# Kernel tuning notes

Measured on AMD Instinct MI355X. Metric: run time of the kernel, lower is better.

Reference implementation:

```python
import jax, jax.numpy as jnp
import numpy as np

N_NODES = 100000
N_EDGES = 1600000
D = 128


def setup_inputs() -> dict:
    key = jax.random.key(0)
    ks = jax.random.split(key, 10)
    s = 1.0 / np.sqrt(D)
    return {
        "feat": jax.random.normal(ks[0], (N_NODES, D), dtype=jnp.float32),
        "W_self0": jax.random.normal(ks[1], (D, D), dtype=jnp.float32) * s,
        "W_neigh0": jax.random.normal(ks[2], (D, D), dtype=jnp.float32) * s,
        "b0": jnp.zeros((D,), dtype=jnp.float32),
        "W_self1": jax.random.normal(ks[3], (D, D), dtype=jnp.float32) * s,
        "W_neigh1": jax.random.normal(ks[4], (D, D), dtype=jnp.float32) * s,
        "b1": jnp.zeros((D,), dtype=jnp.float32),
        "ln_g": jnp.ones((D,), dtype=jnp.float32),
        "ln_b": jnp.zeros((D,), dtype=jnp.float32),
        "edge_src": jax.random.randint(ks[5], (N_EDGES,), 0, N_NODES, dtype=jnp.int32),
        "edge_dst": jax.random.randint(ks[6], (N_EDGES,), 0, N_NODES, dtype=jnp.int32),
        "in_deg": jax.random.randint(ks[7], (N_NODES,), 1, 64, dtype=jnp.int32),
    }


def _sage_layer(h, src, dst, inv_deg, W_self, W_neigh, b):
    # mean aggregation over incoming neighbors: gather -> segment_sum -> scale
    msg = jax.ops.segment_sum(h[src], dst, num_segments=N_NODES)  # [N, d]
    h_neigh = msg * inv_deg[:, None]
    return h @ W_self + h_neigh @ W_neigh + b


def _layer_norm(x, g, b, eps=1e-5):
    mu = jnp.mean(x, axis=-1, keepdims=True)
    var = jnp.mean((x - mu) ** 2, axis=-1, keepdims=True)
    return (x - mu) * jax.lax.rsqrt(var + eps) * g + b


def reference(feat, W_self0, W_neigh0, b0, W_self1, W_neigh1, b1, ln_g, ln_b,
              edge_src, edge_dst, in_deg):
    # Eval mode: dropout = identity, no EmbeddingSelector / reg loss.
    inv_deg = 1.0 / jnp.maximum(in_deg, 1).astype(feat.dtype)
    h = _sage_layer(feat, edge_src, edge_dst, inv_deg, W_self0, W_neigh0, b0)
    h = _layer_norm(h, ln_g, ln_b)
    h = jax.nn.relu(h)
    h = _sage_layer(h, edge_src, edge_dst, inv_deg, W_self1, W_neigh1, b1)
    return h
```

## Files before the change

kernel.cpp:

```cpp
#include <hip/hip_runtime.h>

#define D 128
#define NN 100000
#define PB 391
#define EPB 4096
#define PREP_BLKS 12756

typedef __attribute__((ext_vector_type(8))) short short8;
typedef __attribute__((ext_vector_type(16))) float floatx16;
typedef __attribute__((ext_vector_type(2))) float floatx2;

__device__ inline unsigned short bf16_rne(float f) {
    unsigned int u = __float_as_uint(f);
    u += 0x7fff + ((u >> 16) & 1);
    return (unsigned short)(u >> 16);
}
__device__ inline unsigned char fp8_enc1(float f) {
    return (unsigned char)(__builtin_amdgcn_cvt_pk_fp8_f32(f, f, 0, false) & 0xff);
}


__global__ __launch_bounds__(256) void prep_count_kernel(
    const float* __restrict__ feat, unsigned short* __restrict__ feat16,
    unsigned char* __restrict__ feat8,
    const float* __restrict__ Ws0, const float* __restrict__ Wn0,
    const float* __restrict__ Ws1, const float* __restrict__ Wn1,
    unsigned short* __restrict__ wt0, unsigned short* __restrict__ wt1,
    const int* __restrict__ dst, unsigned int* __restrict__ bucketCnt,
    unsigned int* __restrict__ blockBase, int E)
{
    __shared__ unsigned int h[PB];
    int bid = blockIdx.x;
    if (bid < 12500) {
        int i = bid * 256 + threadIdx.x;
        float4 v = *(const float4*)(feat + (size_t)i * 4);
        unsigned short u[4] = { bf16_rne(v.x), bf16_rne(v.y), bf16_rne(v.z), bf16_rne(v.w) };
        int n  = i >> 5;
        int d0 = (i & 31) * 4;
        size_t f = (size_t)(n >> 5) * 4096 + (size_t)((d0 >> 3) * 32 + (n & 31)) * 8 + (d0 & 7);
        *(uint2*)(feat16 + f) = *(uint2*)u;
        int w = __builtin_amdgcn_cvt_pk_fp8_f32(v.x, v.y, 0, false);
        w = __builtin_amdgcn_cvt_pk_fp8_f32(v.z, v.w, w, true);
        ((unsigned int*)feat8)[i] = (unsigned int)w;
    } else if (bid < PREP_BLKS) {
        int i = (bid - 12500) * 256 + threadIdx.x;
        int layer = i >> 15;
        int r = i & 32767;
        int n = r >> 8;
        int k = r & 255;
        const float* Ws = layer ? Ws1 : Ws0;
        const float* Wn = layer ? Wn1 : Wn0;
        float v = (k < 128) ? Ws[(size_t)k * 128 + n] : Wn[(size_t)(k - 128) * 128 + n];
        unsigned short* wt = layer ? wt1 : wt0;
        int ct = n >> 5, nn = n & 31;
        int hs = k >> 7, k7 = k & 127;
        int kc = k7 >> 4, hf = (k7 >> 3) & 1, j = k7 & 7;
        int frag = ((((ct * 2 + hs) * 8 + kc) * 2 + hf) * 32 + nn) * 8 + j;
        wt[frag] = bf16_rne(v);
    } else {
        const int b = bid - PREP_BLKS;
        const int t = threadIdx.x;
        for (int i = t; i < PB; i += 256) h[i] = 0;
        __syncthreads();
        const int base = b * EPB;
#pragma unroll
        for (int k = 0; k < EPB / 256; k++) {
            int e = base + k * 256 + t;
            if (e < E) atomicAdd(&h[(unsigned)dst[e] >> 8], 1u);
        }
        __syncthreads();
        for (int i = t; i < PB; i += 256) {
            unsigned int c = h[i];
            unsigned int o = 0;
            if (c) o = atomicAdd(&bucketCnt[i], c);
            blockBase[(size_t)b * PB + i] = o;
        }
    }
}

__global__ __launch_bounds__(512) void part_scan_kernel(
    const unsigned int* __restrict__ bucketCnt, unsigned int* __restrict__ bucketStart,
    int E)
{
    __shared__ unsigned int sd[512];
    int t = threadIdx.x;
    unsigned int v = (t < PB) ? bucketCnt[t] : 0u;
    sd[t] = v; __syncthreads();
    for (int off = 1; off < 512; off <<= 1) {
        unsigned int x = (t >= off) ? sd[t - off] : 0u;
        __syncthreads();
        sd[t] += x;
        __syncthreads();
    }
    if (t < PB) bucketStart[t] = sd[t] - v;
    if (t == 0) bucketStart[PB] = (unsigned int)E;
}

__global__ __launch_bounds__(256) void part_scatter_kernel(
    const int* __restrict__ src, const int* __restrict__ dst,
    const unsigned int* __restrict__ bucketStart,
    const unsigned int* __restrict__ blockBase,
    unsigned int* __restrict__ pairs, int E)
{
    __shared__ unsigned int h[PB];
    const int t = threadIdx.x;
    const int b = blockIdx.x;
    for (int i = t; i < PB; i += 256) h[i] = 0;
    __syncthreads();
    const int base = b * EPB;
#pragma unroll
    for (int k = 0; k < EPB / 256; k++) {
        int e = base + k * 256 + t;
        if (e < E) {
            unsigned int d = (unsigned int)dst[e];
            unsigned int bk = d >> 8;
            unsigned int lr = atomicAdd(&h[bk], 1u);
            unsigned int pos = bucketStart[bk] + blockBase[(size_t)b * PB + bk] + lr;
            pairs[pos] = ((unsigned int)src[e] << 8) | (d & 255u);
        }
    }
}

__global__ __launch_bounds__(256) void part_fine_kernel(
    const unsigned int* __restrict__ pairs, const unsigned int* __restrict__ bucketStart,
    int* __restrict__ row_ptr, int* __restrict__ col, int N, int E)
{
    __shared__ unsigned int h[256], sc[256], pos[256];
    const int t = threadIdx.x;
    const int b = blockIdx.x;
    h[t] = 0;
    __syncthreads();
    const unsigned int ebeg = bucketStart[b];
    const unsigned int eend = bucketStart[b + 1];
    for (unsigned int i = ebeg + t; i < eend; i += 256)
        atomicAdd(&h[pairs[i] & 255u], 1u);
    __syncthreads();
    sc[t] = h[t]; __syncthreads();
    for (int off = 1; off < 256; off <<= 1) {
        unsigned int x = (t >= off) ? sc[t - off] : 0u;
        __syncthreads();
        sc[t] += x;
        __syncthreads();
    }
    unsigned int excl = sc[t] - h[t];
    int node = b * 256 + t;
    if (node < N) row_ptr[node] = (int)(ebeg + excl);
    pos[t] = ebeg + excl;
    if (b == 0 && t == 0) row_ptr[N] = E;
    __syncthreads();
    for (unsigned int i = ebeg + t; i < eend; i += 256) {
        unsigned int p = pairs[i];
        unsigned int w = atomicAdd(&pos[p & 255u], 1u);
        col[w] = (int)(p >> 8);
    }
}

__global__ __launch_bounds__(256) void gather8_kernel(
    const unsigned char* __restrict__ h8, const int* __restrict__ row_ptr,
    const int* __restrict__ col, const int* __restrict__ in_deg,
    unsigned short* __restrict__ msg16, int N)
{
    const int wave = threadIdx.x >> 6;
    const int lane = threadIdx.x & 63;
    const int quad = lane >> 4;
    const int ln16 = lane & 15;
    const int node = (blockIdx.x * 4 + wave) * 4 + quad;
    if (node >= N) return;

    const size_t lo = (size_t)ln16 * 8;
    int beg = row_ptr[node];
    int end = row_ptr[node + 1];

    float f[8] = {0.f,0.f,0.f,0.f,0.f,0.f,0.f,0.f};
    int j = beg;
    for (; j + 4 <= end; j += 4) {
        int c0 = col[j], c1 = col[j + 1], c2 = col[j + 2], c3 = col[j + 3];
        uint2 u0 = *(const uint2*)(h8 + (size_t)c0 * D + lo);
        uint2 u1 = *(const uint2*)(h8 + (size_t)c1 * D + lo);
        uint2 u2 = *(const uint2*)(h8 + (size_t)c2 * D + lo);
        uint2 u3 = *(const uint2*)(h8 + (size_t)c3 * D + lo);
#pragma unroll
        for (int q = 0; q < 4; q++) {
            uint2 u = q == 0 ? u0 : q == 1 ? u1 : q == 2 ? u2 : u3;
            floatx2 p0 = __builtin_amdgcn_cvt_pk_f32_fp8((int)u.x, false);
            floatx2 p1 = __builtin_amdgcn_cvt_pk_f32_fp8((int)u.x, true);
            floatx2 p2 = __builtin_amdgcn_cvt_pk_f32_fp8((int)u.y, false);
            floatx2 p3 = __builtin_amdgcn_cvt_pk_f32_fp8((int)u.y, true);
            f[0] += p0.x; f[1] += p0.y; f[2] += p1.x; f[3] += p1.y;
            f[4] += p2.x; f[5] += p2.y; f[6] += p3.x; f[7] += p3.y;
        }
    }
    for (; j < end; ++j) {
        uint2 u = *(const uint2*)(h8 + (size_t)col[j] * D + lo);
        floatx2 p0 = __builtin_amdgcn_cvt_pk_f32_fp8((int)u.x, false);
        floatx2 p1 = __builtin_amdgcn_cvt_pk_f32_fp8((int)u.x, true);
        floatx2 p2 = __builtin_amdgcn_cvt_pk_f32_fp8((int)u.y, false);
        floatx2 p3 = __builtin_amdgcn_cvt_pk_f32_fp8((int)u.y, true);
        f[0] += p0.x; f[1] += p0.y; f[2] += p1.x; f[3] += p1.y;
        f[4] += p2.x; f[5] += p2.y; f[6] += p3.x; f[7] += p3.y;
    }
    int dg = in_deg[node];
    float invd = 1.f / (float)(dg > 1 ? dg : 1);
    unsigned short us[8];
#pragma unroll
    for (int i = 0; i < 8; i++) us[i] = bf16_rne(f[i] * invd);
    size_t fo = (size_t)(node >> 5) * 4096 + ((size_t)ln16 * 32 + (node & 31)) * 8;
    *(uint4*)(msg16 + fo) = *(const uint4*)us;
}

__global__ __launch_bounds__(256, 3) void mfma32_kernel(
    const unsigned short* __restrict__ A16, const unsigned short* __restrict__ Msg16,
    const unsigned short* __restrict__ Wt,
    const float* __restrict__ bias,
    const float* __restrict__ ln_g, const float* __restrict__ ln_b,
    unsigned short* __restrict__ Out16, unsigned char* __restrict__ Out8,
    float* __restrict__ Out32, int N, int do_ln)
{
    __shared__ char smem[49152];

    const int tid  = threadIdx.x;
    const int wave = tid >> 6;
    const int lane = tid & 63;
    const int half = lane >> 5;
    const int n32  = lane & 31;
    const int brow0 = blockIdx.x * 128;
    const int wrow0 = brow0 + wave * 32;

    const int NT = N >> 5;
    int tile = wrow0 >> 5;
    if (tile >= NT) tile = NT - 1;
    const short8* Af = (const short8*)(A16   + (size_t)tile * 4096);
    const short8* Mf = (const short8*)(Msg16 + (size_t)tile * 4096);

    floatx16 acc[4];
#pragma unroll
    for (int ct = 0; ct < 4; ct++)
#pragma unroll
        for (int r = 0; r < 16; r++) acc[ct][r] = 0.f;

#pragma unroll
    for (int hs = 0; hs < 2; hs++) {
        const short8* Sf = hs ? Mf : Af;
#pragma unroll
        for (int kc = 0; kc < 8; kc++) {
            short8 a = Sf[kc * 64 + lane];
#pragma unroll
            for (int ct = 0; ct < 4; ct++) {
                short8 b = *(const short8*)(Wt + ((size_t)((ct * 2 + hs) * 8 + kc) * 64 + lane) * 8);
                acc[ct] = __builtin_amdgcn_mfma_f32_32x32x16_bf16(a, b, acc[ct], 0, 0, 0);
            }
        }
    }

    float bb[4];
#pragma unroll
    for (int ct = 0; ct < 4; ct++) bb[ct] = bias[ct * 32 + n32];

    float v[4][16];
#pragma unroll
    for (int ct = 0; ct < 4; ct++)
#pragma unroll
        for (int r = 0; r < 16; r++) v[ct][r] = acc[ct][r] + bb[ct];

    if (do_ln) {
        float gg[4], be[4];
#pragma unroll
        for (int ct = 0; ct < 4; ct++) {
            gg[ct] = ln_g[ct * 32 + n32];
            be[ct] = ln_b[ct * 32 + n32];
        }
        float s[16], s2[16];
#pragma unroll
        for (int r = 0; r < 16; r++) {
            s[r]  = v[0][r] + v[1][r] + v[2][r] + v[3][r];
            s2[r] = v[0][r]*v[0][r] + v[1][r]*v[1][r] + v[2][r]*v[2][r] + v[3][r]*v[3][r];
        }
#pragma unroll
        for (int off = 1; off < 32; off <<= 1) {
#pragma unroll
            for (int r = 0; r < 16; r++) {
                s[r]  += __shfl_xor(s[r],  off);
                s2[r] += __shfl_xor(s2[r], off);
            }
        }
        unsigned char* sO8 = (unsigned char*)smem + 32768;
#pragma unroll
        for (int r = 0; r < 16; r++) {
            float mean = s[r] * (1.f / 128.f);
            float var  = s2[r] * (1.f / 128.f) - mean * mean;
            float rstd = rsqrtf(var + 1e-5f);
            int brow = wave * 32 + (r & 3) + 8 * (r >> 2) + 4 * half;
#pragma unroll
            for (int ct = 0; ct < 4; ct++) {
                float t = (v[ct][r] - mean) * rstd * gg[ct] + be[ct];
                t = t > 0.f ? t : 0.f;
                int slot = (ct * 4 + (n32 >> 3)) ^ (brow & 15);
                *(unsigned short*)(smem + brow * 256 + slot * 16 + (n32 & 7) * 2) = bf16_rne(t);
                sO8[brow * 128 + ct * 32 + n32] = fp8_enc1(t);
            }
        }
        __syncthreads();
#pragma unroll
        for (int i = 0; i < 8; i++) {
            int ch = tid + i * 256;
            int tl = ch >> 9, p = ch & 511, kc2 = p >> 5, rr = p & 31;
            if (brow0 + tl * 32 + rr < N)
                *(uint4*)(Out16 + (size_t)brow0 * D + ch * 8) =
                    *(const uint4*)&smem[(tl * 32 + rr) * 256 + ((kc2 ^ (rr & 15)) * 16)];
        }
#pragma unroll
        for (int i = 0; i < 4; i++) {
            int ch = tid + i * 256;
            if (brow0 + (ch >> 3) < N)
                *(uint4*)(Out8 + (size_t)brow0 * D + ch * 16) = *(const uint4*)&sO8[ch * 16];
        }
    } else {
#pragma unroll
        for (int r = 0; r < 16; r++) {
            int row = wrow0 + (r & 3) + 8 * (r >> 2) + 4 * half;
            if (row < N) {
#pragma unroll
                for (int ct = 0; ct < 4; ct++)
                    Out32[(size_t)row * D + ct * 32 + n32] = v[ct][r];
            }
        }
    }
}

extern "C" void kernel_launch(void* const* d_in, const int* in_sizes, int n_in,
                              void* d_out, int out_size, void* d_ws, size_t ws_size,
                              hipStream_t stream)
{
    const float* feat = (const float*)d_in[0];
    const float* Ws0  = (const float*)d_in[1];
    const float* Wn0  = (const float*)d_in[2];
    const float* b0   = (const float*)d_in[3];
    const float* Ws1  = (const float*)d_in[4];
    const float* Wn1  = (const float*)d_in[5];
    const float* b1   = (const float*)d_in[6];
    const float* lng  = (const float*)d_in[7];
    const float* lnb  = (const float*)d_in[8];
    const int* esrc   = (const int*)d_in[9];
    const int* edst   = (const int*)d_in[10];
    const int* indeg  = (const int*)d_in[11];

    const int N = NN;
    const int E = in_sizes[9];

    float* out = (float*)d_out;

    const int nblk = (E + EPB - 1) / EPB;
    char* ws = (char*)d_ws;
    size_t o = 0;
    auto alloc = [&](size_t bytes) { char* p = ws + o; o += (bytes + 15) & ~(size_t)15; return p; };
    unsigned short* feat16 = (unsigned short*)alloc((size_t)N * D * 2);
    int* col     = (int*)alloc((size_t)E * 4);
    int* row_ptr = (int*)alloc((size_t)(N + 1) * 4);
    unsigned short* wt0 = (unsigned short*)alloc(128 * 256 * 2);
    unsigned short* wt1 = (unsigned short*)alloc(128 * 256 * 2);
    size_t csr_bytes = (size_t)(512 + 512 + (size_t)nblk * PB + E) * 4 + 64;
    char* regD = alloc((size_t)N * D * 2 > csr_bytes ? (size_t)N * D * 2 : csr_bytes);
    unsigned int* bucketCnt   = (unsigned int*)regD;
    unsigned int* bucketStart = bucketCnt + 512;
    unsigned int* blockBase   = bucketStart + 512;
    unsigned int* pairs       = blockBase + (size_t)nblk * PB;
    unsigned short* h116 = (unsigned short*)regD;

    unsigned short* msg0  = (unsigned short*)d_out;
    unsigned char*  feat8 = (unsigned char*)d_out + (size_t)N * D * 2;
    unsigned char*  h18   = (unsigned char*)d_out + (size_t)N * D * 3;
    unsigned short* msg1  = feat16;
    (void)ws_size;

    const int gemm_blocks = (N + 127) / 128;
    const int gather_blocks = (N + 15) / 16;

    hipMemsetAsync(bucketCnt, 0, 512 * 4, stream);
    prep_count_kernel<<<PREP_BLKS + nblk, 256, 0, stream>>>(
        feat, feat16, feat8, Ws0, Wn0, Ws1, Wn1, wt0, wt1,
        edst, bucketCnt, blockBase, E);

    part_scan_kernel<<<1, 512, 0, stream>>>(bucketCnt, bucketStart, E);
    part_scatter_kernel<<<nblk, 256, 0, stream>>>(esrc, edst, bucketStart, blockBase, pairs, E);
    part_fine_kernel<<<PB, 256, 0, stream>>>(pairs, bucketStart, row_ptr, col, N, E);

    gather8_kernel<<<gather_blocks, 256, 0, stream>>>(feat8, row_ptr, col, indeg, msg0, N);
    mfma32_kernel<<<gemm_blocks, 256, 0, stream>>>(
        feat16, msg0, wt0, b0, lng, lnb, h116, h18, nullptr, N, 1);

    gather8_kernel<<<gather_blocks, 256, 0, stream>>>(h18, row_ptr, col, indeg, msg1, N);
    mfma32_kernel<<<gemm_blocks, 256, 0, stream>>>(
        h116, msg1, wt1, b1, nullptr, nullptr, nullptr, nullptr, out, N, 0);
}
```

Measured before the change: 308.8 us.

## Unroll gather by 8 with packed accumulators and split GEMM into LN and f32 kernels

The neighbour gather now loads eight columns per iteration and accumulates into packed float2 vectors, with an occupancy hint of six blocks per SM, to expose more memory-level parallelism. The GEMM kernel is split into a LayerNorm variant and a plain f32-output variant, so the second layer drops the unused shared memory and runs at a higher occupancy hint. EPB is reduced from 4096 to 1024, which changes how the CSR-build partition kernels split edges across blocks. More unrolling raises register pressure, and the smaller EPB adds more partition blocks.

```diff
diff --git a/kernel.cpp b/kernel.cpp
--- a/kernel.cpp
+++ b/kernel.cpp
@@ -3,7 +3,7 @@
 #define D 128
 #define NN 100000
 #define PB 391
-#define EPB 4096
+#define EPB 1024
 #define PREP_BLKS 12756
 
 typedef __attribute__((ext_vector_type(8))) short short8;
@@ -155,24 +155,44 @@
     }
 }
 
-__global__ __launch_bounds__(256) void gather8_kernel(
+__global__ __launch_bounds__(256, 6) void gather16f_kernel(
     const unsigned char* __restrict__ h8, const int* __restrict__ row_ptr,
     const int* __restrict__ col, const int* __restrict__ in_deg,
     unsigned short* __restrict__ msg16, int N)
 {
-    const int wave = threadIdx.x >> 6;
-    const int lane = threadIdx.x & 63;
-    const int quad = lane >> 4;
-    const int ln16 = lane & 15;
-    const int node = (blockIdx.x * 4 + wave) * 4 + quad;
+    const int tid  = threadIdx.x;
+    const int nq   = tid >> 4;
+    const int ln16 = tid & 15;
+    const int node = blockIdx.x * 16 + nq;
     if (node >= N) return;
-
     const size_t lo = (size_t)ln16 * 8;
+
     int beg = row_ptr[node];
     int end = row_ptr[node + 1];
 
-    float f[8] = {0.f,0.f,0.f,0.f,0.f,0.f,0.f,0.f};
+    floatx2 a0 = {0.f, 0.f}, a1 = {0.f, 0.f}, a2 = {0.f, 0.f}, a3 = {0.f, 0.f};
     int j = beg;
+    for (; j + 8 <= end; j += 8) {
+        int c0 = col[j],     c1 = col[j + 1], c2 = col[j + 2], c3 = col[j + 3];
+        int c4 = col[j + 4], c5 = col[j + 5], c6 = col[j + 6], c7 = col[j + 7];
+        uint2 u0 = *(const uint2*)(h8 + (size_t)c0 * D + lo);
+        uint2 u1 = *(const uint2*)(h8 + (size_t)c1 * D + lo);
+        uint2 u2 = *(const uint2*)(h8 + (size_t)c2 * D + lo);
+        uint2 u3 = *(const uint2*)(h8 + (size_t)c3 * D + lo);
+        uint2 u4 = *(const uint2*)(h8 + (size_t)c4 * D + lo);
+        uint2 u5 = *(const uint2*)(h8 + (size_t)c5 * D + lo);
+        uint2 u6 = *(const uint2*)(h8 + (size_t)c6 * D + lo);
+        uint2 u7 = *(const uint2*)(h8 + (size_t)c7 * D + lo);
+#pragma unroll
+        for (int q = 0; q < 8; q++) {
+            uint2 u = q == 0 ? u0 : q == 1 ? u1 : q == 2 ? u2 : q == 3 ? u3
+                    : q == 4 ? u4 : q == 5 ? u5 : q == 6 ? u6 : u7;
+            a0 += __builtin_amdgcn_cvt_pk_f32_fp8((int)u.x, false);
+            a1 += __builtin_amdgcn_cvt_pk_f32_fp8((int)u.x, true);
+            a2 += __builtin_amdgcn_cvt_pk_f32_fp8((int)u.y, false);
+            a3 += __builtin_amdgcn_cvt_pk_f32_fp8((int)u.y, true);
+        }
+    }
     for (; j + 4 <= end; j += 4) {
         int c0 = col[j], c1 = col[j + 1], c2 = col[j + 2], c3 = col[j + 3];
         uint2 u0 = *(const uint2*)(h8 + (size_t)c0 * D + lo);
@@ -182,39 +202,38 @@
 #pragma unroll
         for (int q = 0; q < 4; q++) {
             uint2 u = q == 0 ? u0 : q == 1 ? u1 : q == 2 ? u2 : u3;
-            floatx2 p0 = __builtin_amdgcn_cvt_pk_f32_fp8((int)u.x, false);
-            floatx2 p1 = __builtin_amdgcn_cvt_pk_f32_fp8((int)u.x, true);
-            floatx2 p2 = __builtin_amdgcn_cvt_pk_f32_fp8((int)u.y, false);
-            floatx2 p3 = __builtin_amdgcn_cvt_pk_f32_fp8((int)u.y, true);
-            f[0] += p0.x; f[1] += p0.y; f[2] += p1.x; f[3] += p1.y;
-            f[4] += p2.x; f[5] += p2.y; f[6] += p3.x; f[7] += p3.y;
+            a0 += __builtin_amdgcn_cvt_pk_f32_fp8((int)u.x, false);
+            a1 += __builtin_amdgcn_cvt_pk_f32_fp8((int)u.x, true);
+            a2 += __builtin_amdgcn_cvt_pk_f32_fp8((int)u.y, false);
+            a3 += __builtin_amdgcn_cvt_pk_f32_fp8((int)u.y, true);
         }
     }
     for (; j < end; ++j) {
         uint2 u = *(const uint2*)(h8 + (size_t)col[j] * D + lo);
-        floatx2 p0 = __builtin_amdgcn_cvt_pk_f32_fp8((int)u.x, false);
-        floatx2 p1 = __builtin_amdgcn_cvt_pk_f32_fp8((int)u.x, true);
-        floatx2 p2 = __builtin_amdgcn_cvt_pk_f32_fp8((int)u.y, false);
-        floatx2 p3 = __builtin_amdgcn_cvt_pk_f32_fp8((int)u.y, true);
-        f[0] += p0.x; f[1] += p0.y; f[2] += p1.x; f[3] += p1.y;
-        f[4] += p2.x; f[5] += p2.y; f[6] += p3.x; f[7] += p3.y;
-    }
+        a0 += __builtin_amdgcn_cvt_pk_f32_fp8((int)u.x, false);
+        a1 += __builtin_amdgcn_cvt_pk_f32_fp8((int)u.x, true);
+        a2 += __builtin_amdgcn_cvt_pk_f32_fp8((int)u.y, false);
+        a3 += __builtin_amdgcn_cvt_pk_f32_fp8((int)u.y, true);
+    }
+
     int dg = in_deg[node];
     float invd = 1.f / (float)(dg > 1 ? dg : 1);
     unsigned short us[8];
-#pragma unroll
-    for (int i = 0; i < 8; i++) us[i] = bf16_rne(f[i] * invd);
+    us[0] = bf16_rne(a0.x * invd); us[1] = bf16_rne(a0.y * invd);
+    us[2] = bf16_rne(a1.x * invd); us[3] = bf16_rne(a1.y * invd);
+    us[4] = bf16_rne(a2.x * invd); us[5] = bf16_rne(a2.y * invd);
+    us[6] = bf16_rne(a3.x * invd); us[7] = bf16_rne(a3.y * invd);
     size_t fo = (size_t)(node >> 5) * 4096 + ((size_t)ln16 * 32 + (node & 31)) * 8;
     *(uint4*)(msg16 + fo) = *(const uint4*)us;
 }
 
-__global__ __launch_bounds__(256, 3) void mfma32_kernel(
+__global__ __launch_bounds__(256, 3) void mfma32_ln_kernel(
     const unsigned short* __restrict__ A16, const unsigned short* __restrict__ Msg16,
     const unsigned short* __restrict__ Wt,
     const float* __restrict__ bias,
     const float* __restrict__ ln_g, const float* __restrict__ ln_b,
     unsigned short* __restrict__ Out16, unsigned char* __restrict__ Out8,
-    float* __restrict__ Out32, int N, int do_ln)
+    int N)
 {
     __shared__ char smem[49152];
 
@@ -252,77 +271,117 @@
         }
     }
 
+    float bb[4], gg[4], be[4];
+#pragma unroll
+    for (int ct = 0; ct < 4; ct++) {
+        bb[ct] = bias[ct * 32 + n32];
+        gg[ct] = ln_g[ct * 32 + n32];
+        be[ct] = ln_b[ct * 32 + n32];
+    }
+    float v[4][16];
+#pragma unroll
+    for (int ct = 0; ct < 4; ct++)
+#pragma unroll
+        for (int r = 0; r < 16; r++) v[ct][r] = acc[ct][r] + bb[ct];
+
+    float s[16], s2[16];
+#pragma unroll
+    for (int r = 0; r < 16; r++) {
+        s[r]  = v[0][r] + v[1][r] + v[2][r] + v[3][r];
+        s2[r] = v[0][r]*v[0][r] + v[1][r]*v[1][r] + v[2][r]*v[2][r] + v[3][r]*v[3][r];
+    }
+#pragma unroll
+    for (int off = 1; off < 32; off <<= 1) {
+#pragma unroll
+        for (int r = 0; r < 16; r++) {
+            s[r]  += __shfl_xor(s[r],  off);
+            s2[r] += __shfl_xor(s2[r], off);
+        }
+    }
+    unsigned char* sO8 = (unsigned char*)smem + 32768;
+#pragma unroll
+    for (int r = 0; r < 16; r++) {
+        float mean = s[r] * (1.f / 128.f);
+        float var  = s2[r] * (1.f / 128.f) - mean * mean;
+        float rstd = rsqrtf(var + 1e-5f);
+        int brow = wave * 32 + (r & 3) + 8 * (r >> 2) + 4 * half;
+#pragma unroll
+        for (int ct = 0; ct < 4; ct++) {
+            float t = (v[ct][r] - mean) * rstd * gg[ct] + be[ct];
+            t = t > 0.f ? t : 0.f;
+            int slot = (ct * 4 + (n32 >> 3)) ^ (brow & 15);
+            *(unsigned short*)(smem + brow * 256 + slot * 16 + (n32 & 7) * 2) = bf16_rne(t);
+            sO8[brow * 128 + ct * 32 + n32] = fp8_enc1(t);
+        }
+    }
+    __syncthreads();
+#pragma unroll
+    for (int i = 0; i < 8; i++) {
+        int ch = tid + i * 256;
+        int tl = ch >> 9, p = ch & 511, kc2 = p >> 5, rr = p & 31;
+        if (brow0 + tl * 32 + rr < N)
+            *(uint4*)(Out16 + (size_t)brow0 * D + ch * 8) =
+                *(const uint4*)&smem[(tl * 32 + rr) * 256 + ((kc2 ^ (rr & 15)) * 16)];
+    }
+#pragma unroll
+    for (int i = 0; i < 4; i++) {
+        int ch = tid + i * 256;
+        if (brow0 + (ch >> 3) < N)
+            *(uint4*)(Out8 + (size_t)brow0 * D + ch * 16) = *(const uint4*)&sO8[ch * 16];
+    }
+}
+
+__global__ __launch_bounds__(256, 4) void mfma32_f32_kernel(
+    const unsigned short* __restrict__ A16, const unsigned short* __restrict__ Msg16,
+    const unsigned short* __restrict__ Wt,
+    const float* __restrict__ bias,
+    float* __restrict__ Out32, int N)
+{
+    const int tid  = threadIdx.x;
+    const int wave = tid >> 6;
+    const int lane = tid & 63;
+    const int half = lane >> 5;
+    const int n32  = lane & 31;
+    const int brow0 = blockIdx.x * 128;
+    const int wrow0 = brow0 + wave * 32;
+
+    const int NT = N >> 5;
+    int tile = wrow0 >> 5;
+    if (tile >= NT) tile = NT - 1;
+    const short8* Af = (const short8*)(A16   + (size_t)tile * 4096);
+    const short8* Mf = (const short8*)(Msg16 + (size_t)tile * 4096);
+
+    floatx16 acc[4];
+#pragma unroll
+    for (int ct = 0; ct < 4; ct++)
+#pragma unroll
+        for (int r = 0; r < 16; r++) acc[ct][r] = 0.f;
+
+#pragma unroll
+    for (int hs = 0; hs < 2; hs++) {
+        const short8* Sf = hs ? Mf : Af;
+#pragma unroll
+        for (int kc = 0; kc < 8; kc++) {
+            short8 a = Sf[kc * 64 + lane];
+#pragma unroll
+            for (int ct = 0; ct < 4; ct++) {
+                short8 b = *(const short8*)(Wt + ((size_t)((ct * 2 + hs) * 8 + kc) * 64 + lane) * 8);
+                acc[ct] = __builtin_amdgcn_mfma_f32_32x32x16_bf16(a, b, acc[ct], 0, 0, 0);
+            }
+        }
+    }
+
     float bb[4];
 #pragma unroll
     for (int ct = 0; ct < 4; ct++) bb[ct] = bias[ct * 32 + n32];
 
-    float v[4][16];
-#pragma unroll
-    for (int ct = 0; ct < 4; ct++)
-#pragma unroll
-        for (int r = 0; r < 16; r++) v[ct][r] = acc[ct][r] + bb[ct];
-
-    if (do_ln) {
-        float gg[4], be[4];
-#pragma unroll
-        for (int ct = 0; ct < 4; ct++) {
-            gg[ct] = ln_g[ct * 32 + n32];
-            be[ct] = ln_b[ct * 32 + n32];
-        }
-        float s[16], s2[16];
-#pragma unroll
-        for (int r = 0; r < 16; r++) {
-            s[r]  = v[0][r] + v[1][r] + v[2][r] + v[3][r];
-            s2[r] = v[0][r]*v[0][r] + v[1][r]*v[1][r] + v[2][r]*v[2][r] + v[3][r]*v[3][r];
-        }
-#pragma unroll
-        for (int off = 1; off < 32; off <<= 1) {
-#pragma unroll
-            for (int r = 0; r < 16; r++) {
-                s[r]  += __shfl_xor(s[r],  off);
-                s2[r] += __shfl_xor(s2[r], off);
-            }
-        }
-        unsigned char* sO8 = (unsigned char*)smem + 32768;
-#pragma unroll
-        for (int r = 0; r < 16; r++) {
-            float mean = s[r] * (1.f / 128.f);
-            float var  = s2[r] * (1.f / 128.f) - mean * mean;
-            float rstd = rsqrtf(var + 1e-5f);
-            int brow = wave * 32 + (r & 3) + 8 * (r >> 2) + 4 * half;
-#pragma unroll
-            for (int ct = 0; ct < 4; ct++) {
-                float t = (v[ct][r] - mean) * rstd * gg[ct] + be[ct];
-                t = t > 0.f ? t : 0.f;
-                int slot = (ct * 4 + (n32 >> 3)) ^ (brow & 15);
-                *(unsigned short*)(smem + brow * 256 + slot * 16 + (n32 & 7) * 2) = bf16_rne(t);
-                sO8[brow * 128 + ct * 32 + n32] = fp8_enc1(t);
-            }
-        }
-        __syncthreads();
-#pragma unroll
-        for (int i = 0; i < 8; i++) {
-            int ch = tid + i * 256;
-            int tl = ch >> 9, p = ch & 511, kc2 = p >> 5, rr = p & 31;
-            if (brow0 + tl * 32 + rr < N)
-                *(uint4*)(Out16 + (size_t)brow0 * D + ch * 8) =
-                    *(const uint4*)&smem[(tl * 32 + rr) * 256 + ((kc2 ^ (rr & 15)) * 16)];
-        }
-#pragma unroll
-        for (int i = 0; i < 4; i++) {
-            int ch = tid + i * 256;
-            if (brow0 + (ch >> 3) < N)
-                *(uint4*)(Out8 + (size_t)brow0 * D + ch * 16) = *(const uint4*)&sO8[ch * 16];
-        }
-    } else {
-#pragma unroll
-        for (int r = 0; r < 16; r++) {
-            int row = wrow0 + (r & 3) + 8 * (r >> 2) + 4 * half;
-            if (row < N) {
-#pragma unroll
-                for (int ct = 0; ct < 4; ct++)
-                    Out32[(size_t)row * D + ct * 32 + n32] = v[ct][r];
-            }
+#pragma unroll
+    for (int r = 0; r < 16; r++) {
+        int row = wrow0 + (r & 3) + 8 * (r >> 2) + 4 * half;
+        if (row < N) {
+#pragma unroll
+            for (int ct = 0; ct < 4; ct++)
+                Out32[(size_t)row * D + ct * 32 + n32] = acc[ct][r] + bb[ct];
         }
     }
 }
@@ -369,11 +428,11 @@
     unsigned short* msg0  = (unsigned short*)d_out;
     unsigned char*  feat8 = (unsigned char*)d_out + (size_t)N * D * 2;
     unsigned char*  h18   = (unsigned char*)d_out + (size_t)N * D * 3;
-    unsigned short* msg1  = feat16;
+    unsigned short* msg1F = feat16;
     (void)ws_size;
 
     const int gemm_blocks = (N + 127) / 128;
-    const int gather_blocks = (N + 15) / 16;
+    const int g16_blocks  = (N + 15) / 16;
 
     hipMemsetAsync(bucketCnt, 0, 512 * 4, stream);
     prep_count_kernel<<<PREP_BLKS + nblk, 256, 0, stream>>>(
@@ -384,11 +443,10 @@
     part_scatter_kernel<<<nblk, 256, 0, stream>>>(esrc, edst, bucketStart, blockBase, pairs, E);
     part_fine_kernel<<<PB, 256, 0, stream>>>(pairs, bucketStart, row_ptr, col, N, E);
 
-    gather8_kernel<<<gather_blocks, 256, 0, stream>>>(feat8, row_ptr, col, indeg, msg0, N);
-    mfma32_kernel<<<gemm_blocks, 256, 0, stream>>>(
-        feat16, msg0, wt0, b0, lng, lnb, h116, h18, nullptr, N, 1);
-
-    gather8_kernel<<<gather_blocks, 256, 0, stream>>>(h18, row_ptr, col, indeg, msg1, N);
-    mfma32_kernel<<<gemm_blocks, 256, 0, stream>>>(
-        h116, msg1, wt1, b1, nullptr, nullptr, nullptr, nullptr, out, N, 0);
-}
+    gather16f_kernel<<<g16_blocks, 256, 0, stream>>>(feat8, row_ptr, col, indeg, msg0, N);
+    mfma32_ln_kernel<<<gemm_blocks, 256, 0, stream>>>(
+        feat16, msg0, wt0, b0, lng, lnb, h116, h18, N);
+
+    gather16f_kernel<<<g16_blocks, 256, 0, stream>>>(h18, row_ptr, col, indeg, msg1F, N);
+    mfma32_f32_kernel<<<gemm_blocks, 256, 0, stream>>>(h116, msg1F, wt1, b1, out, N);
+}
```

New measurement: 359.3 us. 1.16x slower.
